# Kernel tuning notes

Hardware: AMD Instinct MI355X
Metric: run time of the kernel (lower is better)

The kernel has to match this reference:

```python
import jax, jax.numpy as jnp
import numpy as np

B, D, K, M1, M2 = 256, 128, 32, 64, 32   # batch, n_nodes, K copies, dims[1], dims[2]
H1, H2, L = 128, 64, 32                   # pivae_dims


def setup_inputs() -> dict:
    key = jax.random.key(0)
    ks = iter(jax.random.split(key, 32))

    def rn(shape, scale):
        return jax.random.normal(next(ks), shape, dtype=jnp.float32) * scale

    x = jax.random.normal(next(ks), (B, D), dtype=jnp.float32)

    # per-node fc1 weights: [D, M1, D]; bounds force nonneg with zero diag column
    W1_pos = jnp.abs(rn((D, M1, D), 1.0 / np.sqrt(D)))
    W1_neg = jnp.abs(rn((D, M1, D), 1.0 / np.sqrt(D)))
    eye = jnp.eye(D, dtype=jnp.float32)[:, None, :]   # zero out W[j,:,j]
    W1_pos = W1_pos * (1.0 - eye)
    W1_neg = W1_neg * (1.0 - eye)
    b1_pos = rn((D, M1), 0.02)
    b1_neg = rn((D, M1), 0.02)

    # LocallyConnected stacks: weight [K, m_in, m_out]
    lc1_w = rn((K, M1, M2), 1.0 / np.sqrt(M1)); lc1_b = rn((K, M2), 0.02)
    lc2_w = rn((K, M2, 1), 1.0 / np.sqrt(M2));  lc2_b = rn((K, 1), 0.02)

    # per-sample beta Linear(k,1): weights [B, K], bias [B]
    beta_w = rn((B, K), 1.0 / np.sqrt(K)); beta_b = rn((B,), 0.02)

    # VAE params (encoder -> mu/logvar -> decoder), stored as (in,out) matrices
    enc1_w = rn((K, H1), 1.0 / np.sqrt(K));  enc1_b = jnp.zeros((H1,), jnp.float32)
    enc2_w = rn((H1, H2), 1.0 / np.sqrt(H1)); enc2_b = jnp.zeros((H2,), jnp.float32)
    mu_w = rn((H2, L), 1.0 / np.sqrt(H2));    mu_b = jnp.zeros((L,), jnp.float32)
    lv_w = rn((H2, L), 1.0 / np.sqrt(H2));    lv_b = jnp.zeros((L,), jnp.float32)
    dec1_w = rn((L, H2), 1.0 / np.sqrt(L));   dec1_b = jnp.zeros((H2,), jnp.float32)
    dec2_w = rn((H2, H1), 1.0 / np.sqrt(H2)); dec2_b = jnp.zeros((H1,), jnp.float32)
    dec3_w = rn((H1, K), 1.0 / np.sqrt(H1));  dec3_b = jnp.zeros((K,), jnp.float32)

    eps = jax.random.normal(next(ks), (B, L), dtype=jnp.float32)  # reparam noise

    return dict(x=x, W1_pos=W1_pos, W1_neg=W1_neg, b1_pos=b1_pos, b1_neg=b1_neg,
                lc1_w=lc1_w, lc1_b=lc1_b, lc2_w=lc2_w, lc2_b=lc2_b,
                beta_w=beta_w, beta_b=beta_b,
                enc1_w=enc1_w, enc1_b=enc1_b, enc2_w=enc2_w, enc2_b=enc2_b,
                mu_w=mu_w, mu_b=mu_b, lv_w=lv_w, lv_b=lv_b,
                dec1_w=dec1_w, dec1_b=dec1_b, dec2_w=dec2_w, dec2_b=dec2_b,
                dec3_w=dec3_w, dec3_b=dec3_b, eps=eps)


def reference(x, W1_pos, W1_neg, b1_pos, b1_neg, lc1_w, lc1_b, lc2_w, lc2_b,
              beta_w, beta_b, enc1_w, enc1_b, enc2_w, enc2_b, mu_w, mu_b,
              lv_w, lv_b, dec1_w, dec1_b, dec2_w, dec2_b, dec3_w, dec3_b, eps):
    b, d = x.shape
    k = lc1_w.shape[0]

    # fused per-node fc1: (pos - neg) applied to x with column j zeroed, all j at once
    W1 = W1_pos - W1_neg                      # [D, M1, D]
    b1 = b1_pos - b1_neg                      # [D, M1]
    full = jnp.einsum('bi,jhi->bjh', x, W1)   # as if no column were zeroed
    diagW = jnp.einsum('jhj->jh', W1)         # [D, M1] column-j weight of node j
    phi = full - x[:, :, None] * diagW[None] + b1[None]   # [B, D, M1]

    # expand to K copies, run sigmoid + LocallyConnected stack
    h = jnp.broadcast_to(phi[:, :, None, :], (b, d, k, phi.shape[-1]))
    h = jnp.einsum('bdkm,kmn->bdkn', jax.nn.sigmoid(h), lc1_w) + lc1_b   # [B,D,K,M2]
    h = jnp.einsum('bdkm,kmn->bdkn', jax.nn.sigmoid(h), lc2_w) + lc2_b   # [B,D,K,1]
    last_phi_x = h[..., 0]                    # [B, D, K]

    # per-sample beta projection (batched over B)
    y1 = jnp.einsum('bdk,bk->bd', last_phi_x, beta_w) + beta_b[:, None]

    # VAE on the stacked beta weights [B, K]
    e = jax.nn.relu(beta_w @ enc1_w + enc1_b)
    e = jax.nn.relu(e @ enc2_w + enc2_b)
    mu = e @ mu_w + mu_b
    logvar = e @ lv_w + lv_b
    z = mu + eps * jnp.exp(0.5 * logvar)
    dh = jax.nn.relu(z @ dec1_w + dec1_b)
    dh = jax.nn.relu(dh @ dec2_w + dec2_b)
    recon = dh @ dec3_w + dec3_b              # [B, K]

    y2 = jnp.einsum('bdk,bk->bd', last_phi_x, recon) + beta_b[:, None]
    return (y1, y2, mu, logvar)
```

## Files before the change

### kernel.cpp

```cpp
#include <hip/hip_runtime.h>
#include <stdint.h>

#define BB 256
#define DD 128
#define KK 32
#define MM1 64
#define MM2 32

typedef __attribute__((ext_vector_type(8))) short bf16x8;
typedef __attribute__((ext_vector_type(4))) float f32x4;

#define LOG2E 1.44269504088896f


__device__ __forceinline__ short f2b(float f) {
  uint32_t u = __builtin_bit_cast(uint32_t, f);
  u += 0x7FFFu + ((u >> 16) & 1u);
  return (short)(u >> 16);
}
__device__ __forceinline__ float sigm_pre(float acc, float cpre) {
  return __builtin_amdgcn_rcpf(
      1.0f + __builtin_amdgcn_exp2f(fmaf(acc, -LOG2E, cpre)));
}

__global__ __launch_bounds__(256) void combo_kernel(
    const float* __restrict__ x, const float* __restrict__ W1p,
    const float* __restrict__ W1n, const float* __restrict__ b1p,
    const float* __restrict__ b1n, const float* __restrict__ lc1w,
    const float* __restrict__ lc1b, const float* __restrict__ lc2b,
    const float* __restrict__ betaw,
    const float* __restrict__ enc1w, const float* __restrict__ enc1b,
    const float* __restrict__ enc2w, const float* __restrict__ enc2b,
    const float* __restrict__ muw,  const float* __restrict__ mub,
    const float* __restrict__ lvw,  const float* __restrict__ lvb,
    const float* __restrict__ dec1w, const float* __restrict__ dec1b,
    const float* __restrict__ dec2w, const float* __restrict__ dec2b,
    const float* __restrict__ dec3w, const float* __restrict__ dec3b,
    const float* __restrict__ eps,
    char* __restrict__ ws, float* __restrict__ mu_out,
    float* __restrict__ lv_out)
{
  const int bx = blockIdx.x;
  if (bx < 1024) {
    const int tid = bx * 256 + threadIdx.x;
    {
      float4 a = ((const float4*)W1p)[tid];
      float4 b = ((const float4*)W1n)[tid];
      short4 s;
      s.x = f2b(a.x - b.x); s.y = f2b(a.y - b.y);
      s.z = f2b(a.z - b.z); s.w = f2b(a.w - b.w);
      ((short4*)(ws + 303104))[tid] = s;
    }
    if (tid < 8192) {
      float4 v = ((const float4*)x)[tid];
      short4 s;
      s.x = f2b(v.x); s.y = f2b(v.y); s.z = f2b(v.z); s.w = f2b(v.w);
      ((short4*)(ws + 65536))[tid] = s;
    }
    if (tid < 65536) {
      int k = tid >> 11, n = (tid >> 6) & 31, m = tid & 63;
      ((short*)(ws + 131072))[tid] = f2b(lc1w[k * 2048 + m * 32 + n]);
    }
    if (tid < 8192) {
      ((float*)(ws + 32768))[tid] = betaw[(tid & 255) * 32 + (tid >> 8)];
    }
    if (tid < 1024) { ((float*)(ws + 262144))[tid] = -lc1b[tid] * LOG2E; }
    if (tid < 32) { ((float*)(ws + 266240))[tid] = 0.25f * lc2b[tid]; }
    if (tid < 8192) {
      ((float*)(ws + 270336))[tid] = -(b1p[tid] - b1n[tid]) * LOG2E;
    }
    return;
  }

  const int b = bx - 1024, t = threadIdx.x;
  float* reconT = (float*)ws;
  __shared__ float bw[KK], e1[128], e2[64], zz[32], d1s[64], d2s[128];
  if (t < KK) bw[t] = betaw[b * KK + t];
  __syncthreads();
  if (t < 128) {
    float a0 = enc1b[t], a1 = 0.f;
    #pragma unroll
    for (int k = 0; k < KK; k += 2) {
      a0 = fmaf(bw[k], enc1w[k * 128 + t], a0);
      a1 = fmaf(bw[k + 1], enc1w[(k + 1) * 128 + t], a1);
    }
    e1[t] = fmaxf(a0 + a1, 0.f);
  }
  __syncthreads();
  if (t < 64) {
    float a0 = enc2b[t], a1 = 0.f, a2 = 0.f, a3 = 0.f;
    #pragma unroll 8
    for (int h = 0; h < 128; h += 4) {
      a0 = fmaf(e1[h], enc2w[h * 64 + t], a0);
      a1 = fmaf(e1[h + 1], enc2w[(h + 1) * 64 + t], a1);
      a2 = fmaf(e1[h + 2], enc2w[(h + 2) * 64 + t], a2);
      a3 = fmaf(e1[h + 3], enc2w[(h + 3) * 64 + t], a3);
    }
    e2[t] = fmaxf((a0 + a1) + (a2 + a3), 0.f);
  }
  __syncthreads();
  if (t < 32) {
    float m0 = mub[t], m1 = 0.f, l0 = lvb[t], l1 = 0.f;
    #pragma unroll 8
    for (int h = 0; h < 64; h += 2) {
      float ea = e2[h], eb = e2[h + 1];
      m0 = fmaf(ea, muw[h * 32 + t], m0);
      m1 = fmaf(eb, muw[(h + 1) * 32 + t], m1);
      l0 = fmaf(ea, lvw[h * 32 + t], l0);
      l1 = fmaf(eb, lvw[(h + 1) * 32 + t], l1);
    }
    float m = m0 + m1, l = l0 + l1;
    mu_out[b * 32 + t] = m;
    lv_out[b * 32 + t] = l;
    zz[t] = fmaf(eps[b * 32 + t], __expf(0.5f * l), m);
  }
  __syncthreads();
  if (t < 64) {
    float a0 = dec1b[t], a1 = 0.f;
    #pragma unroll
    for (int l = 0; l < 32; l += 2) {
      a0 = fmaf(zz[l], dec1w[l * 64 + t], a0);
      a1 = fmaf(zz[l + 1], dec1w[(l + 1) * 64 + t], a1);
    }
    d1s[t] = fmaxf(a0 + a1, 0.f);
  }
  __syncthreads();
  if (t < 128) {
    float a0 = dec2b[t], a1 = 0.f, a2 = 0.f, a3 = 0.f;
    #pragma unroll 8
    for (int h = 0; h < 64; h += 4) {
      a0 = fmaf(d1s[h], dec2w[h * 128 + t], a0);
      a1 = fmaf(d1s[h + 1], dec2w[(h + 1) * 128 + t], a1);
      a2 = fmaf(d1s[h + 2], dec2w[(h + 2) * 128 + t], a2);
      a3 = fmaf(d1s[h + 3], dec2w[(h + 3) * 128 + t], a3);
    }
    d2s[t] = fmaxf((a0 + a1) + (a2 + a3), 0.f);
  }
  __syncthreads();
  if (t < 32) {
    float a0 = dec3b[t], a1 = 0.f, a2 = 0.f, a3 = 0.f;
    #pragma unroll 8
    for (int h = 0; h < 128; h += 4) {
      a0 = fmaf(d2s[h], dec3w[h * 32 + t], a0);
      a1 = fmaf(d2s[h + 1], dec3w[(h + 1) * 32 + t], a1);
      a2 = fmaf(d2s[h + 2], dec3w[(h + 2) * 32 + t], a2);
      a3 = fmaf(d2s[h + 3], dec3w[(h + 3) * 32 + t], a3);
    }
    reconT[t * BB + b] = (a0 + a1) + (a2 + a3);
  }
}

__global__ __launch_bounds__(512, 4) void main_kernel(
    const float* __restrict__ lc2w, const float* __restrict__ betab,
    const char* __restrict__ ws, float* __restrict__ out)
{
  const int bx = blockIdx.x;
  const int d = bx >> 2;
  const int bh = bx & 3;
  const int tid = threadIdx.x;
  const int wave = tid >> 6, lane = tid & 63;
  const int g = lane >> 4, l15 = lane & 15;

  const short* __restrict__ xbf   = (const short*)(ws + 65536);
  const short* __restrict__ lc1T  = (const short*)(ws + 131072);
  const float* __restrict__ lc1bs = (const float*)(ws + 262144);
  const float* __restrict__ lc2bq = (const float*)(ws + 266240);
  const float* __restrict__ b1s   = (const float*)(ws + 270336) + d * MM1;
  const short* __restrict__ w1bf  = (const short*)(ws + 303104) + d * (MM1 * DD);
  const float* __restrict__ betaT = (const float*)(ws + 32768);
  const float* __restrict__ recT  = (const float*)(ws + 0);

  __shared__ __align__(16) short sS[64 * 64];
  __shared__ __align__(16) float cS[1024];
  __shared__ __align__(16) float wS[1024];
  __shared__ float lbq[32];
  __shared__ float yred[8][64][2];

  if (tid < 256)      ((f32x4*)cS)[tid]       = ((const f32x4*)lc1bs)[tid];
  else if (tid < 512) ((f32x4*)wS)[tid - 256] = ((const f32x4*)lc2w)[tid - 256];
  if (tid < 32) lbq[tid] = lc2bq[tid];

  bf16x8 Af[4][2][2];
  #pragma unroll
  for (int kk = 0; kk < 4; ++kk)
    #pragma unroll
    for (int nh = 0; nh < 2; ++nh)
      #pragma unroll
      for (int mh = 0; mh < 2; ++mh)
        Af[kk][nh][mh] = *(const bf16x8*)(
            lc1T + ((wave * 4 + kk) * 32 + nh * 16 + l15) * 64 + mh * 32 + g * 8);

  {
    const int rt1 = wave >> 1, mt0 = (wave & 1) * 2;
    bf16x8 xa[4];
    #pragma unroll
    for (int ks = 0; ks < 4; ++ks)
      xa[ks] = *(const bf16x8*)(
          xbf + (bh * 64 + rt1 * 16 + l15) * DD + ks * 32 + g * 8);
    #pragma unroll
    for (int mi = 0; mi < 2; ++mi) {
      const int m = (mt0 + mi) * 16 + l15;
      f32x4 acc = {0.f, 0.f, 0.f, 0.f};
      #pragma unroll
      for (int ks = 0; ks < 4; ++ks) {
        bf16x8 wb = *(const bf16x8*)(w1bf + m * DD + ks * 32 + g * 8);
        acc = __builtin_amdgcn_mfma_f32_16x16x32_bf16(xa[ks], wb, acc, 0, 0, 0);
      }
      const float cpre = b1s[m];
      #pragma unroll
      for (int r = 0; r < 4; ++r) {
        const int bl = rt1 * 16 + g * 4 + r;
        sS[bl * 64 + ((m & ~7) ^ ((bl & 7) << 3)) + (m & 7)] =
            f2b(sigm_pre(acc[r], cpre));
      }
    }
  }
  __syncthreads();

  float y1p[4] = {0, 0, 0, 0}, y2p[4] = {0, 0, 0, 0};
  #pragma unroll
  for (int rt = 0; rt < 4; ++rt) {
    const int b = rt * 16 + l15;
    const int bsw = (b & 7) << 3;
    const bf16x8 sa0 = *(const bf16x8*)&sS[b * 64 + ((g * 8) ^ bsw)];
    const bf16x8 sa1 = *(const bf16x8*)&sS[b * 64 + ((32 + g * 8) ^ bsw)];
    f32x4 acc[4][2];
    #pragma unroll
    for (int kk = 0; kk < 4; ++kk)
      #pragma unroll
      for (int nh = 0; nh < 2; ++nh) {
        f32x4 a = {0.f, 0.f, 0.f, 0.f};
        a = __builtin_amdgcn_mfma_f32_16x16x32_bf16(Af[kk][nh][0], sa0, a, 0, 0, 0);
        a = __builtin_amdgcn_mfma_f32_16x16x32_bf16(Af[kk][nh][1], sa1, a, 0, 0, 0);
        acc[kk][nh] = a;
      }
    const int gb = bh * 64 + b;
    #pragma unroll
    for (int kk = 0; kk < 4; ++kk) {
      const int k = wave * 4 + kk;
      float v = lbq[k];
      #pragma unroll
      for (int nh = 0; nh < 2; ++nh) {
        const f32x4 c4 = *(const f32x4*)&cS[k * 32 + nh * 16 + g * 4];
        const f32x4 w4 = *(const f32x4*)&wS[k * 32 + nh * 16 + g * 4];
        #pragma unroll
        for (int r = 0; r < 4; ++r)
          v = fmaf(sigm_pre(acc[kk][nh][r], c4[r]), w4[r], v);
      }
      y1p[rt] = fmaf(v, betaT[k * BB + gb], y1p[rt]);
      y2p[rt] = fmaf(v, recT[k * BB + gb], y2p[rt]);
    }
  }

  #pragma unroll
  for (int rt = 0; rt < 4; ++rt) {
    y1p[rt] += __shfl_xor(y1p[rt], 16, 64);
    y1p[rt] += __shfl_xor(y1p[rt], 32, 64);
    y2p[rt] += __shfl_xor(y2p[rt], 16, 64);
    y2p[rt] += __shfl_xor(y2p[rt], 32, 64);
  }
  if (g == 0) {
    #pragma unroll
    for (int rt = 0; rt < 4; ++rt) {
      yred[wave][rt * 16 + l15][0] = y1p[rt];
      yred[wave][rt * 16 + l15][1] = y2p[rt];
    }
  }
  __syncthreads();
  if (tid < 128) {
    const int bl = tid >> 1, o = tid & 1;
    float s = 0.f;
    #pragma unroll
    for (int w = 0; w < 8; ++w) s += yred[w][bl][o];
    const int b = bh * 64 + bl;
    out[o * (BB * DD) + b * DD + d] = s + betab[b];
  }
}

extern "C" void kernel_launch(void* const* d_in, const int* in_sizes, int n_in,
                              void* d_out, int out_size, void* d_ws, size_t ws_size,
                              hipStream_t stream) {
  const float* x     = (const float*)d_in[0];
  const float* W1p   = (const float*)d_in[1];
  const float* W1n   = (const float*)d_in[2];
  const float* b1p   = (const float*)d_in[3];
  const float* b1n   = (const float*)d_in[4];
  const float* lc1w  = (const float*)d_in[5];
  const float* lc1b  = (const float*)d_in[6];
  const float* lc2w  = (const float*)d_in[7];
  const float* lc2b  = (const float*)d_in[8];
  const float* betaw = (const float*)d_in[9];
  const float* betab = (const float*)d_in[10];
  const float* enc1w = (const float*)d_in[11];
  const float* enc1b = (const float*)d_in[12];
  const float* enc2w = (const float*)d_in[13];
  const float* enc2b = (const float*)d_in[14];
  const float* muw   = (const float*)d_in[15];
  const float* mub   = (const float*)d_in[16];
  const float* lvw   = (const float*)d_in[17];
  const float* lvb   = (const float*)d_in[18];
  const float* dec1w = (const float*)d_in[19];
  const float* dec1b = (const float*)d_in[20];
  const float* dec2w = (const float*)d_in[21];
  const float* dec2b = (const float*)d_in[22];
  const float* dec3w = (const float*)d_in[23];
  const float* dec3b = (const float*)d_in[24];
  const float* eps   = (const float*)d_in[25];

  float* out    = (float*)d_out;
  char*  ws     = (char*)d_ws;
  float* mu_out = out + BB * DD * 2;
  float* lv_out = mu_out + BB * 32;

  combo_kernel<<<dim3(1280), dim3(256), 0, stream>>>(
      x, W1p, W1n, b1p, b1n, lc1w, lc1b, lc2b, betaw,
      enc1w, enc1b, enc2w, enc2b, muw, mub, lvw, lvb,
      dec1w, dec1b, dec2w, dec2b, dec3w, dec3b, eps,
      ws, mu_out, lv_out);

  main_kernel<<<dim3(512), dim3(512), 0, stream>>>(
      lc2w, betab, (const char*)ws, out);
}
```

Measured before the change: 150.4 us.

## Process two nodes per 1024-thread block and stream lc1 fragments per k

The main kernel now uses 1024-thread blocks, each handling two nodes d for one batch quarter, which halves the grid to 256 blocks. Each half of the waves computes its own sigmoid tile. The loop order is inverted so the lc1 weight fragments, biases and lc2 weights are loaded from global memory per k step instead of being kept in registers and staged in LDS. This is meant to cut register pressure and shared-memory staging, at the cost of more global/L2 loads and fewer, larger blocks, which may reduce occupancy flexibility.

```diff
diff --git a/kernel.cpp b/kernel.cpp
--- a/kernel.cpp
+++ b/kernel.cpp
@@ -150,105 +150,100 @@
   }
 }
 
-__global__ __launch_bounds__(512, 4) void main_kernel(
+__global__ __launch_bounds__(1024) void main_kernel(
     const float* __restrict__ lc2w, const float* __restrict__ betab,
     const char* __restrict__ ws, float* __restrict__ out)
 {
   const int bx = blockIdx.x;
-  const int d = bx >> 2;
-  const int bh = bx & 3;
+  const int d2 = bx >> 2;
+  const int bq = bx & 3;
   const int tid = threadIdx.x;
-  const int wave = tid >> 6, lane = tid & 63;
+  const int wv = tid >> 6, lane = tid & 63;
   const int g = lane >> 4, l15 = lane & 15;
 
   const short* __restrict__ xbf   = (const short*)(ws + 65536);
   const short* __restrict__ lc1T  = (const short*)(ws + 131072);
   const float* __restrict__ lc1bs = (const float*)(ws + 262144);
   const float* __restrict__ lc2bq = (const float*)(ws + 266240);
-  const float* __restrict__ b1s   = (const float*)(ws + 270336) + d * MM1;
-  const short* __restrict__ w1bf  = (const short*)(ws + 303104) + d * (MM1 * DD);
+  const float* __restrict__ b1s   = (const float*)(ws + 270336);
+  const short* __restrict__ w1bf  = (const short*)(ws + 303104);
   const float* __restrict__ betaT = (const float*)(ws + 32768);
   const float* __restrict__ recT  = (const float*)(ws + 0);
 
-  __shared__ __align__(16) short sS[64 * 64];
-  __shared__ __align__(16) float cS[1024];
-  __shared__ __align__(16) float wS[1024];
-  __shared__ float lbq[32];
-  __shared__ float yred[8][64][2];
-
-  if (tid < 256)      ((f32x4*)cS)[tid]       = ((const f32x4*)lc1bs)[tid];
-  else if (tid < 512) ((f32x4*)wS)[tid - 256] = ((const f32x4*)lc2w)[tid - 256];
-  if (tid < 32) lbq[tid] = lc2bq[tid];
-
-  bf16x8 Af[4][2][2];
-  #pragma unroll
-  for (int kk = 0; kk < 4; ++kk)
-    #pragma unroll
-    for (int nh = 0; nh < 2; ++nh)
-      #pragma unroll
-      for (int mh = 0; mh < 2; ++mh)
-        Af[kk][nh][mh] = *(const bf16x8*)(
-            lc1T + ((wave * 4 + kk) * 32 + nh * 16 + l15) * 64 + mh * 32 + g * 8);
+  __shared__ __align__(16) short sS[2][64 * 64];
+  __shared__ float yred[16][64][2];
+
+  const int dsel = wv >> 3;
+  const int d = d2 * 2 + dsel;
 
   {
-    const int rt1 = wave >> 1, mt0 = (wave & 1) * 2;
+    const int sub = wv & 7;
+    const int bt = sub >> 1, mtp = (sub & 1) * 2;
+    const short* xrow = xbf + (bq * 64 + bt * 16 + l15) * DD + g * 8;
     bf16x8 xa[4];
     #pragma unroll
     for (int ks = 0; ks < 4; ++ks)
-      xa[ks] = *(const bf16x8*)(
-          xbf + (bh * 64 + rt1 * 16 + l15) * DD + ks * 32 + g * 8);
+      xa[ks] = *(const bf16x8*)(xrow + ks * 32);
+    const short* wrow = w1bf + d * (MM1 * DD);
     #pragma unroll
     for (int mi = 0; mi < 2; ++mi) {
-      const int m = (mt0 + mi) * 16 + l15;
+      const int m = (mtp + mi) * 16 + l15;
       f32x4 acc = {0.f, 0.f, 0.f, 0.f};
       #pragma unroll
       for (int ks = 0; ks < 4; ++ks) {
-        bf16x8 wb = *(const bf16x8*)(w1bf + m * DD + ks * 32 + g * 8);
+        bf16x8 wb = *(const bf16x8*)(wrow + m * DD + ks * 32 + g * 8);
         acc = __builtin_amdgcn_mfma_f32_16x16x32_bf16(xa[ks], wb, acc, 0, 0, 0);
       }
-      const float cpre = b1s[m];
+      const float cpre = b1s[d * MM1 + m];
       #pragma unroll
       for (int r = 0; r < 4; ++r) {
-        const int bl = rt1 * 16 + g * 4 + r;
-        sS[bl * 64 + ((m & ~7) ^ ((bl & 7) << 3)) + (m & 7)] =
+        const int bl = bt * 16 + g * 4 + r;
+        sS[dsel][bl * 64 + ((m & ~7) ^ ((bl & 7) << 3)) + (m & 7)] =
             f2b(sigm_pre(acc[r], cpre));
       }
     }
   }
   __syncthreads();
 
+  const int ksel = wv & 7;
   float y1p[4] = {0, 0, 0, 0}, y2p[4] = {0, 0, 0, 0};
+  const short* sbase = sS[dsel];
+
   #pragma unroll
-  for (int rt = 0; rt < 4; ++rt) {
-    const int b = rt * 16 + l15;
-    const int bsw = (b & 7) << 3;
-    const bf16x8 sa0 = *(const bf16x8*)&sS[b * 64 + ((g * 8) ^ bsw)];
-    const bf16x8 sa1 = *(const bf16x8*)&sS[b * 64 + ((32 + g * 8) ^ bsw)];
-    f32x4 acc[4][2];
-    #pragma unroll
-    for (int kk = 0; kk < 4; ++kk)
+  for (int kk = 0; kk < 4; ++kk) {
+    const int k = ksel * 4 + kk;
+    const short* ap = lc1T + (k * 32 + l15) * 64 + g * 8;
+    const bf16x8 A00 = *(const bf16x8*)(ap);
+    const bf16x8 A01 = *(const bf16x8*)(ap + 32);
+    const bf16x8 A10 = *(const bf16x8*)(ap + 16 * 64);
+    const bf16x8 A11 = *(const bf16x8*)(ap + 16 * 64 + 32);
+    const f32x4 c40 = *(const f32x4*)(lc1bs + k * 32 + g * 4);
+    const f32x4 c41 = *(const f32x4*)(lc1bs + k * 32 + 16 + g * 4);
+    const f32x4 w40 = *(const f32x4*)(lc2w + k * 32 + g * 4);
+    const f32x4 w41 = *(const f32x4*)(lc2w + k * 32 + 16 + g * 4);
+    const float lb = lc2bq[k];
+    const float* bTk = betaT + k * BB + bq * 64 + l15;
+    const float* rTk = recT + k * BB + bq * 64 + l15;
+
+    #pragma unroll
+    for (int rt = 0; rt < 4; ++rt) {
+      const int b = rt * 16 + l15;
+      const int bsw = (b & 7) << 3;
+      const bf16x8 sa0 = *(const bf16x8*)&sbase[b * 64 + ((g * 8) ^ bsw)];
+      const bf16x8 sa1 = *(const bf16x8*)&sbase[b * 64 + ((32 + g * 8) ^ bsw)];
+      f32x4 a0 = {0.f, 0.f, 0.f, 0.f}, a1 = {0.f, 0.f, 0.f, 0.f};
+      a0 = __builtin_amdgcn_mfma_f32_16x16x32_bf16(A00, sa0, a0, 0, 0, 0);
+      a0 = __builtin_amdgcn_mfma_f32_16x16x32_bf16(A01, sa1, a0, 0, 0, 0);
+      a1 = __builtin_amdgcn_mfma_f32_16x16x32_bf16(A10, sa0, a1, 0, 0, 0);
+      a1 = __builtin_amdgcn_mfma_f32_16x16x32_bf16(A11, sa1, a1, 0, 0, 0);
+      float v = lb;
       #pragma unroll
-      for (int nh = 0; nh < 2; ++nh) {
-        f32x4 a = {0.f, 0.f, 0.f, 0.f};
-        a = __builtin_amdgcn_mfma_f32_16x16x32_bf16(Af[kk][nh][0], sa0, a, 0, 0, 0);
-        a = __builtin_amdgcn_mfma_f32_16x16x32_bf16(Af[kk][nh][1], sa1, a, 0, 0, 0);
-        acc[kk][nh] = a;
+      for (int r = 0; r < 4; ++r) {
+        v = fmaf(sigm_pre(a0[r], c40[r]), w40[r], v);
+        v = fmaf(sigm_pre(a1[r], c41[r]), w41[r], v);
       }
-    const int gb = bh * 64 + b;
-    #pragma unroll
-    for (int kk = 0; kk < 4; ++kk) {
-      const int k = wave * 4 + kk;
-      float v = lbq[k];
-      #pragma unroll
-      for (int nh = 0; nh < 2; ++nh) {
-        const f32x4 c4 = *(const f32x4*)&cS[k * 32 + nh * 16 + g * 4];
-        const f32x4 w4 = *(const f32x4*)&wS[k * 32 + nh * 16 + g * 4];
-        #pragma unroll
-        for (int r = 0; r < 4; ++r)
-          v = fmaf(sigm_pre(acc[kk][nh][r], c4[r]), w4[r], v);
-      }
-      y1p[rt] = fmaf(v, betaT[k * BB + gb], y1p[rt]);
-      y2p[rt] = fmaf(v, recT[k * BB + gb], y2p[rt]);
+      y1p[rt] = fmaf(v, bTk[rt * 16], y1p[rt]);
+      y2p[rt] = fmaf(v, rTk[rt * 16], y2p[rt]);
     }
   }
 
@@ -262,18 +257,18 @@
   if (g == 0) {
     #pragma unroll
     for (int rt = 0; rt < 4; ++rt) {
-      yred[wave][rt * 16 + l15][0] = y1p[rt];
-      yred[wave][rt * 16 + l15][1] = y2p[rt];
-    }
-  }
-  __syncthreads();
-  if (tid < 128) {
-    const int bl = tid >> 1, o = tid & 1;
+      yred[wv][rt * 16 + l15][0] = y1p[rt];
+      yred[wv][rt * 16 + l15][1] = y2p[rt];
+    }
+  }
+  __syncthreads();
+  if (tid < 256) {
+    const int o = tid & 1, bl = (tid >> 1) & 63, ds = tid >> 7;
     float s = 0.f;
     #pragma unroll
-    for (int w = 0; w < 8; ++w) s += yred[w][bl][o];
-    const int b = bh * 64 + bl;
-    out[o * (BB * DD) + b * DD + d] = s + betab[b];
+    for (int j = 0; j < 8; ++j) s += yred[ds * 8 + j][bl][o];
+    const int gb = bq * 64 + bl;
+    out[o * (BB * DD) + gb * DD + d2 * 2 + ds] = s + betab[gb];
   }
 }
 
@@ -318,6 +313,6 @@
       dec1w, dec1b, dec2w, dec2b, dec3w, dec3b, eps,
       ws, mu_out, lv_out);
 
-  main_kernel<<<dim3(512), dim3(512), 0, stream>>>(
+  main_kernel<<<dim3(256), dim3(1024), 0, stream>>>(
       lc2w, betab, (const char*)ws, out);
 }
```

Result: faster. 135.6 us (-9.8%).
